# Kernel tuning notes

Measured on AMD Instinct MI355X. Metric: run time of the kernel, lower is better.

## Reference

```python
import jax, jax.numpy as jnp
import numpy as np

NEG = -9e15

def setup_inputs() -> dict:
    key = jax.random.key(0)
    k_h, k_adj, k_W, k_bW, k_a1, k_b1, k_a2, k_b2 = jax.random.split(key, 8)
    N, IN, OUT = 8192, 512, 512
    h = jax.random.normal(k_h, (N, IN), dtype=jnp.float32)
    adj = jax.random.randint(k_adj, (N, N), 0, 2, dtype=jnp.int32)
    # torch Linear default init: U(-1/sqrt(fan_in), 1/sqrt(fan_in))
    s_in = 1.0 / np.sqrt(IN)
    s_out = 1.0 / np.sqrt(OUT)
    W = jax.random.uniform(k_W, (IN, OUT), minval=-s_in, maxval=s_in, dtype=jnp.float32)
    bW = jax.random.uniform(k_bW, (OUT,), minval=-s_in, maxval=s_in, dtype=jnp.float32)
    a1 = jax.random.uniform(k_a1, (OUT,), minval=-s_out, maxval=s_out, dtype=jnp.float32)
    b1 = jax.random.uniform(k_b1, (), minval=-s_out, maxval=s_out, dtype=jnp.float32)
    a2 = jax.random.uniform(k_a2, (OUT,), minval=-s_out, maxval=s_out, dtype=jnp.float32)
    b2 = jax.random.uniform(k_b2, (), minval=-s_out, maxval=s_out, dtype=jnp.float32)
    return {"h": h, "adj": adj, "W": W, "bW": bW, "a1": a1, "b1": b1, "a2": a2, "b2": b2}

def reference(h, adj, W, bW, a1, b1, a2, b2):
    alpha = 0.2
    # Wh: [N, OUT]; dropout is identity at inference (training=False)
    Wh = h @ W + bW
    Wha1 = Wh @ a1 + b1  # [N]
    Wha2 = Wh @ a2 + b2  # [N]
    e = Wha1[:, None] + Wha2[None, :]  # [N, N] broadcast additive scores
    e = jnp.where(e > 0, e, alpha * e)  # leaky relu
    e = jnp.where(adj > 0, e, jnp.float32(-9e15))
    attention = jax.nn.softmax(e, axis=1)
    h_prime = attention @ Wh  # [N, OUT]
    return h_prime
```

## Files before the change

### kernel.cpp

```cpp
#include <hip/hip_runtime.h>
#include <stdint.h>


#define NN 8192
#define DD 512

typedef __attribute__((ext_vector_type(8))) short short8;
typedef __attribute__((ext_vector_type(4))) float f32x4;
typedef __attribute__((ext_vector_type(4))) float float4v;
typedef __attribute__((ext_vector_type(4))) unsigned short ushort4v;

__device__ __forceinline__ uint16_t f2bf(float f) {
  union { float f; uint32_t u; } v; v.f = f;
  uint32_t u = v.u;
  u += 0x7fffu + ((u >> 16) & 1u);
  return (uint16_t)(u >> 16);
}
__device__ __forceinline__ float bf2f(uint16_t b) {
  union { uint32_t u; float f; } v; v.u = ((uint32_t)b) << 16;
  return v.f;
}

__device__ __forceinline__ void async_copy16(uint16_t* lds, const uint16_t* g) {
  __builtin_amdgcn_global_load_lds(
      (const __attribute__((address_space(1))) uint32_t*)g,
      (__attribute__((address_space(3))) uint32_t*)lds, 16, 0, 0);
}

__global__ __launch_bounds__(256) void conv_wt(const float* __restrict__ W,
                                               uint16_t* __restrict__ WT) {
  __shared__ float ts[64][65];
  int tid = threadIdx.x;
  int kt = (blockIdx.x >> 3) * 64, ct = (blockIdx.x & 7) * 64;
  #pragma unroll
  for (int it = 0; it < 4; ++it) {
    int idx = it * 256 + tid;
    int r = idx >> 4, q = idx & 15;
    float4v v = *(const float4v*)(W + (size_t)(kt + r) * 512 + ct + q * 4);
    ts[r][q * 4 + 0] = v.x; ts[r][q * 4 + 1] = v.y;
    ts[r][q * 4 + 2] = v.z; ts[r][q * 4 + 3] = v.w;
  }
  __syncthreads();
  #pragma unroll
  for (int it = 0; it < 4; ++it) {
    int idx = it * 256 + tid;
    int c = idx >> 4, q = idx & 15;
    ushort4v p;
    p.x = f2bf(ts[q * 4 + 0][c]); p.y = f2bf(ts[q * 4 + 1][c]);
    p.z = f2bf(ts[q * 4 + 2][c]); p.w = f2bf(ts[q * 4 + 3][c]);
    *(ushort4v*)(WT + (size_t)(ct + c) * 512 + kt + q * 4) = p;
  }
}

__global__ __launch_bounds__(512) void wh_gemm(const float* __restrict__ h,
                                               const uint16_t* __restrict__ WT,
                                               const float* __restrict__ bW,
                                               const float* __restrict__ a1,
                                               const float* __restrict__ a2,
                                               uint16_t* __restrict__ WhT,
                                               float* __restrict__ s1g,
                                               float* __restrict__ s2g) {
  __shared__ __align__(16) uint16_t At[32 * 32];
  __shared__ __align__(16) uint16_t Bt[512 * 32];
  __shared__ float s1loc[32], s2loc[32];
  int tid = threadIdx.x;
  int wave = tid >> 6, lane = tid & 63;
  int l15 = lane & 15, quad = lane >> 4;
  int i0 = blockIdx.x * 32;
  if (tid < 32) { s1loc[tid] = 0.f; s2loc[tid] = 0.f; }
  f32x4 acc[2][4] = {};
  for (int k0 = 0; k0 < 512; k0 += 32) {
    if (tid < 256) {
      int r = tid >> 3, ks = (tid & 7) * 4;
      float4v hv = *(const float4v*)(h + (size_t)(i0 + r) * 512 + k0 + ks);
      ushort4v p;
      p.x = f2bf(hv.x); p.y = f2bf(hv.y); p.z = f2bf(hv.z); p.w = f2bf(hv.w);
      *(ushort4v*)&At[r * 32 + ks] = p;
    }
    #pragma unroll
    for (int rr = 0; rr < 4; ++rr) {
      int idx = rr * 512 + tid;
      int c = idx >> 2, q = idx & 3;
      async_copy16(&Bt[idx * 8], WT + c * 512 + k0 + q * 8);
    }
    __syncthreads();
    short8 a0 = *(const short8*)&At[l15 * 32 + quad * 8];
    short8 a1f = *(const short8*)&At[(l15 + 16) * 32 + quad * 8];
    #pragma unroll
    for (int nt = 0; nt < 4; ++nt) {
      int c = wave * 64 + nt * 16 + l15;
      short8 b = *(const short8*)&Bt[c * 32 + quad * 8];
      acc[0][nt] = __builtin_amdgcn_mfma_f32_16x16x32_bf16(a0, b, acc[0][nt], 0, 0, 0);
      acc[1][nt] = __builtin_amdgcn_mfma_f32_16x16x32_bf16(a1f, b, acc[1][nt], 0, 0, 0);
    }
    __syncthreads();
  }
  #pragma unroll
  for (int mt = 0; mt < 2; ++mt) {
    int ib = i0 + mt * 16 + quad * 4;
    float r1[4] = {0.f, 0.f, 0.f, 0.f};
    float r2[4] = {0.f, 0.f, 0.f, 0.f};
    #pragma unroll
    for (int nt = 0; nt < 4; ++nt) {
      int c = wave * 64 + nt * 16 + l15;
      float bias = bW[c];
      float a1c = a1[c], a2c = a2[c];
      float v0 = acc[mt][nt].x + bias;
      float v1 = acc[mt][nt].y + bias;
      float v2 = acc[mt][nt].z + bias;
      float v3 = acc[mt][nt].w + bias;
      ushort4v p;
      p.x = f2bf(v0); p.y = f2bf(v1); p.z = f2bf(v2); p.w = f2bf(v3);
      *(ushort4v*)&WhT[(size_t)c * 8192 + ib] = p;
      r1[0] = fmaf(v0, a1c, r1[0]); r1[1] = fmaf(v1, a1c, r1[1]);
      r1[2] = fmaf(v2, a1c, r1[2]); r1[3] = fmaf(v3, a1c, r1[3]);
      r2[0] = fmaf(v0, a2c, r2[0]); r2[1] = fmaf(v1, a2c, r2[1]);
      r2[2] = fmaf(v2, a2c, r2[2]); r2[3] = fmaf(v3, a2c, r2[3]);
    }
    #pragma unroll
    for (int v = 0; v < 4; ++v) {
      int row = mt * 16 + quad * 4 + v;
      atomicAdd(&s1loc[row], r1[v]);
      atomicAdd(&s2loc[row], r2[v]);
    }
  }
  __syncthreads();
  if (tid < 32) {
    s1g[i0 + tid] = s1loc[tid];
    s2g[i0 + tid] = s2loc[tid];
  }
}

__global__ __launch_bounds__(512, 4) void attn2(const int* __restrict__ adj,
                                                const float* __restrict__ s1,
                                                const float* __restrict__ s2,
                                                const float* __restrict__ b1,
                                                const float* __restrict__ b2,
                                                const uint16_t* __restrict__ WhT,
                                                float* __restrict__ out) {
  __shared__ __align__(16) uint16_t At[32 * 128];
  __shared__ __align__(16) uint16_t Bt[256 * 128];
  __shared__ float dred[512];
  __shared__ float dloc[32];
  int tid = threadIdx.x;
  int wave = tid >> 6, lane = tid & 63;
  int l15 = lane & 15, quad = lane >> 4;
  int x = blockIdx.x;
  int cb = (x >> 3) & 1;
  int rb = (x & 7) | ((x >> 4) << 3);
  int i0 = rb * 32, c0 = cb * 256;
  int wr = tid >> 4, p = tid & 15;
  float s1v = s1[i0 + wr] + b1[0] + b2[0];
  const int* adjp = adj + (size_t)(i0 + wr) * 8192 + p * 8;
  const float* s2p = s2 + p * 8;
  uint16_t* awp = &At[wr * 128 + ((p ^ (wr & 15)) * 8)];
  float dpart = 0.f;
  f32x4 acc[2][2] = {};
  int4 av0 = *(const int4*)(adjp);
  int4 av1 = *(const int4*)(adjp + 4);
  for (int j0 = 0; j0 < 8192; j0 += 128) {
    #pragma unroll
    for (int it = 0; it < 8; ++it) {
      int idx = it * 512 + tid;
      int r = idx >> 4, pp = idx & 15;
      int sc = pp ^ (r & 15);
      async_copy16(&Bt[idx * 8], WhT + (size_t)(c0 + r) * 8192 + j0 + sc * 8);
    }
    int jn = (j0 + 128) & 8191;
    int4 nv0 = *(const int4*)(adjp + jn);
    int4 nv1 = *(const int4*)(adjp + jn + 4);
    float4v sv0 = *(const float4v*)(s2p + j0);
    float4v sv1 = *(const float4v*)(s2p + j0 + 4);
    short8 pk;
    float e, wv;
    uint16_t b;
    e = s1v + sv0.x; e = fmaxf(e, 0.2f * e);
    wv = (av0.x > 0) ? __expf(e) : 0.f; b = f2bf(wv); pk[0] = (short)b; dpart += bf2f(b);
    e = s1v + sv0.y; e = fmaxf(e, 0.2f * e);
    wv = (av0.y > 0) ? __expf(e) : 0.f; b = f2bf(wv); pk[1] = (short)b; dpart += bf2f(b);
    e = s1v + sv0.z; e = fmaxf(e, 0.2f * e);
    wv = (av0.z > 0) ? __expf(e) : 0.f; b = f2bf(wv); pk[2] = (short)b; dpart += bf2f(b);
    e = s1v + sv0.w; e = fmaxf(e, 0.2f * e);
    wv = (av0.w > 0) ? __expf(e) : 0.f; b = f2bf(wv); pk[3] = (short)b; dpart += bf2f(b);
    e = s1v + sv1.x; e = fmaxf(e, 0.2f * e);
    wv = (av1.x > 0) ? __expf(e) : 0.f; b = f2bf(wv); pk[4] = (short)b; dpart += bf2f(b);
    e = s1v + sv1.y; e = fmaxf(e, 0.2f * e);
    wv = (av1.y > 0) ? __expf(e) : 0.f; b = f2bf(wv); pk[5] = (short)b; dpart += bf2f(b);
    e = s1v + sv1.z; e = fmaxf(e, 0.2f * e);
    wv = (av1.z > 0) ? __expf(e) : 0.f; b = f2bf(wv); pk[6] = (short)b; dpart += bf2f(b);
    e = s1v + sv1.w; e = fmaxf(e, 0.2f * e);
    wv = (av1.w > 0) ? __expf(e) : 0.f; b = f2bf(wv); pk[7] = (short)b; dpart += bf2f(b);
    *(short8*)awp = pk;
    av0 = nv0; av1 = nv1;
    __syncthreads();
    int brow0 = wave * 32 + l15;
    int brow1 = brow0 + 16;
    #pragma unroll
    for (int ks = 0; ks < 4; ++ks) {
      int ch = ks * 4 + quad;
      short8 b0 = *(const short8*)&Bt[brow0 * 128 + ((ch ^ l15) * 8)];
      short8 b1f = *(const short8*)&Bt[brow1 * 128 + ((ch ^ l15) * 8)];
      short8 am0 = *(const short8*)&At[l15 * 128 + ((ch ^ l15) * 8)];
      short8 am1 = *(const short8*)&At[(l15 + 16) * 128 + ((ch ^ l15) * 8)];
      acc[0][0] = __builtin_amdgcn_mfma_f32_16x16x32_bf16(am0, b0, acc[0][0], 0, 0, 0);
      acc[0][1] = __builtin_amdgcn_mfma_f32_16x16x32_bf16(am0, b1f, acc[0][1], 0, 0, 0);
      acc[1][0] = __builtin_amdgcn_mfma_f32_16x16x32_bf16(am1, b0, acc[1][0], 0, 0, 0);
      acc[1][1] = __builtin_amdgcn_mfma_f32_16x16x32_bf16(am1, b1f, acc[1][1], 0, 0, 0);
    }
    __syncthreads();
  }
  dred[tid] = dpart;
  __syncthreads();
  if (tid < 32) {
    float s = 0.f;
    #pragma unroll
    for (int q = 0; q < 16; ++q) s += dred[tid * 16 + q];
    dloc[tid] = 1.0f / s;
  }
  __syncthreads();
  #pragma unroll
  for (int mt = 0; mt < 2; ++mt) {
    #pragma unroll
    for (int nt = 0; nt < 2; ++nt) {
      int c = c0 + wave * 32 + nt * 16 + l15;
      #pragma unroll
      for (int v = 0; v < 4; ++v) {
        int row = mt * 16 + quad * 4 + v;
        out[(size_t)(i0 + row) * 512 + c] = acc[mt][nt][v] * dloc[row];
      }
    }
  }
}

extern "C" void kernel_launch(void* const* d_in, const int* in_sizes, int n_in,
                              void* d_out, int out_size, void* d_ws, size_t ws_size,
                              hipStream_t stream) {
  const float* h   = (const float*)d_in[0];
  const int*   adj = (const int*)d_in[1];
  const float* W   = (const float*)d_in[2];
  const float* bW  = (const float*)d_in[3];
  const float* a1  = (const float*)d_in[4];
  const float* b1  = (const float*)d_in[5];
  const float* a2  = (const float*)d_in[6];
  const float* b2  = (const float*)d_in[7];
  float* out = (float*)d_out;
  char* ws = (char*)d_ws;

  uint16_t* WhT = (uint16_t*)(ws);
  uint16_t* WT  = (uint16_t*)(ws + 8388608);
  float* s1     = (float*)(ws + 8912896);
  float* s2     = (float*)(ws + 8945664);

  conv_wt<<<64, 256, 0, stream>>>(W, WT);
  wh_gemm<<<256, 512, 0, stream>>>(h, WT, bW, a1, a2, WhT, s1, s2);
  attn2<<<512, 512, 0, stream>>>(adj, s1, s2, b1, b2, WhT, out);
}
```

Baseline: 548.7 us.

## Precompress adjacency into transposed bitmask to avoid reading int32 adj twice

Adds a pre-pass that packs the int32 adjacency matrix into a per-row bitmask, laid out so each attention thread loads one byte per tile. The attention kernel reads that bitmask instead of re-reading the full int32 adj for each column block, which removes most of the HBM traffic. Block-index mapping is also changed so both column blocks of a row group run close together. The softmax denominator is now summed from fp32 weights rather than bf16-rounded ones, a slight numerics difference.

```diff
diff --git a/kernel.cpp b/kernel.cpp
--- a/kernel.cpp
+++ b/kernel.cpp
@@ -15,10 +15,6 @@
   uint32_t u = v.u;
   u += 0x7fffu + ((u >> 16) & 1u);
   return (uint16_t)(u >> 16);
-}
-__device__ __forceinline__ float bf2f(uint16_t b) {
-  union { uint32_t u; float f; } v; v.u = ((uint32_t)b) << 16;
-  return v.f;
 }
 
 __device__ __forceinline__ void async_copy16(uint16_t* lds, const uint16_t* g) {
@@ -131,7 +127,29 @@
   }
 }
 
-__global__ __launch_bounds__(512, 4) void attn2(const int* __restrict__ adj,
+__global__ __launch_bounds__(256) void adj2b(const int* __restrict__ adj,
+                                             uint8_t* __restrict__ bmT) {
+  int i = blockIdx.x;
+  int t = threadIdx.x;
+  const int* ap = adj + (size_t)i * 8192 + t * 32;
+  uint32_t bits = 0;
+  #pragma unroll
+  for (int q4 = 0; q4 < 8; ++q4) {
+    int4 v = *(const int4*)(ap + q4 * 4);
+    bits |= (v.x > 0 ? 1u : 0u) << (q4 * 4 + 0);
+    bits |= (v.y > 0 ? 1u : 0u) << (q4 * 4 + 1);
+    bits |= (v.z > 0 ? 1u : 0u) << (q4 * 4 + 2);
+    bits |= (v.w > 0 ? 1u : 0u) << (q4 * 4 + 3);
+  }
+  size_t base = (size_t)i * 1024 + (size_t)(t >> 2);
+  int p0 = 4 * (t & 3);
+  bmT[base + (size_t)(p0 + 0) * 64] = (uint8_t)(bits & 0xff);
+  bmT[base + (size_t)(p0 + 1) * 64] = (uint8_t)((bits >> 8) & 0xff);
+  bmT[base + (size_t)(p0 + 2) * 64] = (uint8_t)((bits >> 16) & 0xff);
+  bmT[base + (size_t)(p0 + 3) * 64] = (uint8_t)((bits >> 24) & 0xff);
+}
+
+__global__ __launch_bounds__(512, 4) void attn3(const uint8_t* __restrict__ bmT,
                                                 const float* __restrict__ s1,
                                                 const float* __restrict__ s2,
                                                 const float* __restrict__ b1,
@@ -146,52 +164,46 @@
   int wave = tid >> 6, lane = tid & 63;
   int l15 = lane & 15, quad = lane >> 4;
   int x = blockIdx.x;
-  int cb = (x >> 3) & 1;
-  int rb = (x & 7) | ((x >> 4) << 3);
+  int cb = (x >> 2) & 1;
+  int rb = ((x >> 3) << 2) | (x & 3);
   int i0 = rb * 32, c0 = cb * 256;
   int wr = tid >> 4, p = tid & 15;
   float s1v = s1[i0 + wr] + b1[0] + b2[0];
-  const int* adjp = adj + (size_t)(i0 + wr) * 8192 + p * 8;
+  const uint8_t* bmp = bmT + (size_t)(i0 + wr) * 1024 + p * 64;
   const float* s2p = s2 + p * 8;
   uint16_t* awp = &At[wr * 128 + ((p ^ (wr & 15)) * 8)];
   float dpart = 0.f;
   f32x4 acc[2][2] = {};
-  int4 av0 = *(const int4*)(adjp);
-  int4 av1 = *(const int4*)(adjp + 4);
-  for (int j0 = 0; j0 < 8192; j0 += 128) {
-    #pragma unroll
-    for (int it = 0; it < 8; ++it) {
-      int idx = it * 512 + tid;
+  uint32_t bcur = bmp[0];
+  for (int it = 0; it < 64; ++it) {
+    int j0 = it * 128;
+    #pragma unroll
+    for (int s = 0; s < 8; ++s) {
+      int idx = s * 512 + tid;
       int r = idx >> 4, pp = idx & 15;
       int sc = pp ^ (r & 15);
       async_copy16(&Bt[idx * 8], WhT + (size_t)(c0 + r) * 8192 + j0 + sc * 8);
     }
-    int jn = (j0 + 128) & 8191;
-    int4 nv0 = *(const int4*)(adjp + jn);
-    int4 nv1 = *(const int4*)(adjp + jn + 4);
+    uint32_t bnext = bmp[(it + 1) & 63];
     float4v sv0 = *(const float4v*)(s2p + j0);
     float4v sv1 = *(const float4v*)(s2p + j0 + 4);
+    float e, wf[8];
+    e = s1v + sv0.x; e = fmaxf(e, 0.2f * e); wf[0] = (bcur & 1u)   ? __expf(e) : 0.f;
+    e = s1v + sv0.y; e = fmaxf(e, 0.2f * e); wf[1] = (bcur & 2u)   ? __expf(e) : 0.f;
+    e = s1v + sv0.z; e = fmaxf(e, 0.2f * e); wf[2] = (bcur & 4u)   ? __expf(e) : 0.f;
+    e = s1v + sv0.w; e = fmaxf(e, 0.2f * e); wf[3] = (bcur & 8u)   ? __expf(e) : 0.f;
+    e = s1v + sv1.x; e = fmaxf(e, 0.2f * e); wf[4] = (bcur & 16u)  ? __expf(e) : 0.f;
+    e = s1v + sv1.y; e = fmaxf(e, 0.2f * e); wf[5] = (bcur & 32u)  ? __expf(e) : 0.f;
+    e = s1v + sv1.z; e = fmaxf(e, 0.2f * e); wf[6] = (bcur & 64u)  ? __expf(e) : 0.f;
+    e = s1v + sv1.w; e = fmaxf(e, 0.2f * e); wf[7] = (bcur & 128u) ? __expf(e) : 0.f;
+    dpart += ((wf[0] + wf[1]) + (wf[2] + wf[3])) + ((wf[4] + wf[5]) + (wf[6] + wf[7]));
     short8 pk;
-    float e, wv;
-    uint16_t b;
-    e = s1v + sv0.x; e = fmaxf(e, 0.2f * e);
-    wv = (av0.x > 0) ? __expf(e) : 0.f; b = f2bf(wv); pk[0] = (short)b; dpart += bf2f(b);
-    e = s1v + sv0.y; e = fmaxf(e, 0.2f * e);
-    wv = (av0.y > 0) ? __expf(e) : 0.f; b = f2bf(wv); pk[1] = (short)b; dpart += bf2f(b);
-    e = s1v + sv0.z; e = fmaxf(e, 0.2f * e);
-    wv = (av0.z > 0) ? __expf(e) : 0.f; b = f2bf(wv); pk[2] = (short)b; dpart += bf2f(b);
-    e = s1v + sv0.w; e = fmaxf(e, 0.2f * e);
-    wv = (av0.w > 0) ? __expf(e) : 0.f; b = f2bf(wv); pk[3] = (short)b; dpart += bf2f(b);
-    e = s1v + sv1.x; e = fmaxf(e, 0.2f * e);
-    wv = (av1.x > 0) ? __expf(e) : 0.f; b = f2bf(wv); pk[4] = (short)b; dpart += bf2f(b);
-    e = s1v + sv1.y; e = fmaxf(e, 0.2f * e);
-    wv = (av1.y > 0) ? __expf(e) : 0.f; b = f2bf(wv); pk[5] = (short)b; dpart += bf2f(b);
-    e = s1v + sv1.z; e = fmaxf(e, 0.2f * e);
-    wv = (av1.z > 0) ? __expf(e) : 0.f; b = f2bf(wv); pk[6] = (short)b; dpart += bf2f(b);
-    e = s1v + sv1.w; e = fmaxf(e, 0.2f * e);
-    wv = (av1.w > 0) ? __expf(e) : 0.f; b = f2bf(wv); pk[7] = (short)b; dpart += bf2f(b);
+    pk[0] = (short)f2bf(wf[0]); pk[1] = (short)f2bf(wf[1]);
+    pk[2] = (short)f2bf(wf[2]); pk[3] = (short)f2bf(wf[3]);
+    pk[4] = (short)f2bf(wf[4]); pk[5] = (short)f2bf(wf[5]);
+    pk[6] = (short)f2bf(wf[6]); pk[7] = (short)f2bf(wf[7]);
     *(short8*)awp = pk;
-    av0 = nv0; av1 = nv1;
+    bcur = bnext;
     __syncthreads();
     int brow0 = wave * 32 + l15;
     int brow1 = brow0 + 16;
@@ -250,8 +262,10 @@
   uint16_t* WT  = (uint16_t*)(ws + 8388608);
   float* s1     = (float*)(ws + 8912896);
   float* s2     = (float*)(ws + 8945664);
+  uint8_t* bmT  = (uint8_t*)(ws + 8978432);
 
   conv_wt<<<64, 256, 0, stream>>>(W, WT);
   wh_gemm<<<256, 512, 0, stream>>>(h, WT, bW, a1, a2, WhT, s1, s2);
-  attn2<<<512, 512, 0, stream>>>(adj, s1, s2, b1, b2, WhT, out);
-}
+  adj2b<<<8192, 256, 0, stream>>>(adj, bmT);
+  attn3<<<512, 512, 0, stream>>>(bmT, s1, s2, b1, b2, WhT, out);
+}
```

After: 590.9 us. 7.7% more time.
